# Performance work log

Measured on AMD Instinct MI355X. Metric: run time of the kernel, lower is better.

Reference implementation:

```python
import jax, jax.numpy as jnp
import numpy as np

B, K, N, D, H, DOUT = 16, 8, 196, 768, 3072, 768


def setup_inputs() -> dict:
    key = jax.random.key(0)
    ks = jax.random.split(key, 5)
    scale_w1 = 1.0 / np.sqrt(D)
    scale_w2 = 1.0 / np.sqrt(H)
    return {
        "slots": jax.random.normal(ks[0], (B, K, D), dtype=jnp.float32),
        "pos_embed": jax.random.normal(ks[1], (N, D), dtype=jnp.float32) * 0.02,
        "map_alpha": jax.random.normal(ks[2], (N, DOUT), dtype=jnp.float32) * 0.02,
        "W1": jax.random.normal(ks[3], (D, H), dtype=jnp.float32) * scale_w1,
        "b1": jnp.zeros((H,), dtype=jnp.float32),
        "W2": jax.random.normal(ks[4], (H, DOUT), dtype=jnp.float32) * scale_w2,
        "b2": jnp.zeros((DOUT,), dtype=jnp.float32),
    }


def reference(slots, pos_embed, map_alpha, W1, b1, W2, b2):
    b, k, d = slots.shape
    n = pos_embed.shape[0]
    # broadcast slots over patches and add positional embedding: (B,K,N,D)
    tokens = slots[:, :, None, :] + pos_embed[None, None, :, :]
    # 2-layer MLP with ReLU
    h = jax.nn.relu(jnp.einsum('bknd,dh->bknh', tokens, W1) + b1)
    y_k = jnp.einsum('bknh,ho->bkno', h, W2) + b2  # (B,K,N,DOUT)
    # softmax over K of map_alpha expanded over (B,K); identical across K -> uniform 1/K,
    # computed explicitly for faithfulness to the original module
    m_k = jax.nn.softmax(jnp.broadcast_to(map_alpha[None, None, :, :], (b, k, n, map_alpha.shape[1])), axis=1)
    y = jnp.einsum('bknd,bknd->bnd', y_k, m_k)
    return y
```

## Files before the change

kernel.cpp:

```cpp
#include <hip/hip_runtime.h>
#include <hip/hip_bf16.h>
#include <stdint.h>


typedef __attribute__((ext_vector_type(8))) short bf16x8;
typedef __attribute__((ext_vector_type(4))) float f32x4;

#define AS1 __attribute__((address_space(1)))
#define AS3 __attribute__((address_space(3)))

#define WAIT_VM(N) asm volatile("s_waitcnt vmcnt(" #N ")" ::: "memory")
#define BAR()      asm volatile("s_barrier" ::: "memory")
#define BAR_LDS()  asm volatile("s_waitcnt lgkmcnt(0)\ns_barrier" ::: "memory")

static __device__ __forceinline__ void gld_lds16(const void* g, void* l) {
    __builtin_amdgcn_global_load_lds((const AS1 unsigned int*)g,
                                     (AS3 unsigned int*)l, 16, 0, 0);
}

static __device__ __forceinline__ unsigned short f2bf(float f) {
    union { float f; unsigned int u; } v; v.f = f;
    unsigned int u = v.u;
    return (unsigned short)((u + 0x7fffu + ((u >> 16) & 1u)) >> 16);
}

__global__ void k_prep(const float* __restrict__ W1, unsigned short* __restrict__ W1t,
                       const float* __restrict__ S, const float* __restrict__ P,
                       unsigned short* __restrict__ A1) {
    int idx = blockIdx.x * blockDim.x + threadIdx.x;
    const int C1n = 96 * 3072;
    const int PKn = 96 * 384;
    if (idx < C1n) {
        int r  = idx % 3072;
        int kc = idx / 3072;
        unsigned int po[4];
        #pragma unroll
        for (int j = 0; j < 4; ++j) {
            unsigned short lo = f2bf(W1[(size_t)(kc * 8 + 2 * j) * 3072 + r]);
            unsigned short hi = f2bf(W1[(size_t)(kc * 8 + 2 * j + 1) * 3072 + r]);
            po[j] = (unsigned int)lo | ((unsigned int)hi << 16);
        }
        size_t dst = ((size_t)(r >> 6) * 12 + (kc >> 3)) * 4096
                   + (size_t)((kc & 7) * 64 + (r & 63)) * 8;
        *(uint4*)(W1t + dst) = make_uint4(po[0], po[1], po[2], po[3]);
    } else if (idx < C1n + PKn) {
        int t = idx - C1n;
        int r  = t % 384;
        int kc = t / 384;
        uint4 o = make_uint4(0u, 0u, 0u, 0u);
        if (r < 324) {
            const float* src = (r < 128) ? (S + (size_t)r * 768 + kc * 8)
                                         : (P + (size_t)(r - 128) * 768 + kc * 8);
            float4 a = *(const float4*)(src);
            float4 b = *(const float4*)(src + 4);
            o.x = (unsigned int)f2bf(a.x) | ((unsigned int)f2bf(a.y) << 16);
            o.y = (unsigned int)f2bf(a.z) | ((unsigned int)f2bf(a.w) << 16);
            o.z = (unsigned int)f2bf(b.x) | ((unsigned int)f2bf(b.y) << 16);
            o.w = (unsigned int)f2bf(b.z) | ((unsigned int)f2bf(b.w) << 16);
        }
        size_t dst = ((size_t)(r >> 6) * 12 + (kc >> 3)) * 4096
                   + (size_t)((kc & 7) * 64 + (r & 63)) * 8;
        *(uint4*)(A1 + dst) = o;
    }
}

__launch_bounds__(256)
__global__ void k_gemm1_w2t(const unsigned short* __restrict__ A,
                            const unsigned short* __restrict__ Bt,
                            float* __restrict__ C,
                            const float* __restrict__ W2,
                            unsigned short* __restrict__ W2t) {
    const int tid = threadIdx.x;
    if (blockIdx.x >= 288) {
        int idx = (blockIdx.x - 288) * 256 + tid;
        int r  = idx % 768;
        int kc = idx / 768;
        unsigned int po[4];
        #pragma unroll
        for (int j = 0; j < 4; ++j) {
            unsigned short lo = f2bf(W2[(size_t)(kc * 8 + 2 * j) * 768 + r]);
            unsigned short hi = f2bf(W2[(size_t)(kc * 8 + 2 * j + 1) * 768 + r]);
            po[j] = (unsigned int)lo | ((unsigned int)hi << 16);
        }
        size_t dst = ((size_t)(r >> 6) * 48 + (kc >> 3)) * 4096
                   + (size_t)((kc & 7) * 64 + (r & 63)) * 8;
        *(uint4*)(W2t + dst) = make_uint4(po[0], po[1], po[2], po[3]);
        return;
    }

    __shared__ unsigned short sm[3 * 8192];
    const int lane = tid & 63;
    const int wave = tid >> 6;
    const int wm = wave >> 1, wn = wave & 1;
    const int q = lane >> 4, l16 = lane & 15;

    const int id = blockIdx.x;
    const int j  = id >> 3;
    const int nt = (id & 7) * 6 + j % 6;
    const int rt = j / 6;

    const unsigned short* Ab = A  + (size_t)rt * 12 * 4096;
    const unsigned short* Bb = Bt + (size_t)nt * 12 * 4096;

    f32x4 acc[2][2] = {};
    const int offA = (wm * 32 + l16) * 8;
    const int offB = 4096 + (wn * 32 + l16) * 8;

    auto stage = [&](int i, unsigned short* d) {
        const unsigned short* Ag = Ab + (size_t)i * 4096;
        const unsigned short* Bg = Bb + (size_t)i * 4096;
        gld_lds16(Ag + tid * 8,        d + tid * 8);
        gld_lds16(Ag + 2048 + tid * 8, d + 2048 + tid * 8);
        gld_lds16(Bg + tid * 8,        d + 4096 + tid * 8);
        gld_lds16(Bg + 2048 + tid * 8, d + 6144 + tid * 8);
    };
    auto compute = [&](const unsigned short* buf) {
        #pragma unroll
        for (int ks = 0; ks < 2; ++ks) {
            const int ko = (ks * 4 + q) * 512;
            bf16x8 af0 = *(const bf16x8*)(buf + ko + offA);
            bf16x8 af1 = *(const bf16x8*)(buf + ko + offA + 128);
            bf16x8 bf0 = *(const bf16x8*)(buf + ko + offB);
            bf16x8 bf1 = *(const bf16x8*)(buf + ko + offB + 128);
            acc[0][0] = __builtin_amdgcn_mfma_f32_16x16x32_bf16(af0, bf0, acc[0][0], 0, 0, 0);
            acc[0][1] = __builtin_amdgcn_mfma_f32_16x16x32_bf16(af0, bf1, acc[0][1], 0, 0, 0);
            acc[1][0] = __builtin_amdgcn_mfma_f32_16x16x32_bf16(af1, bf0, acc[1][0], 0, 0, 0);
            acc[1][1] = __builtin_amdgcn_mfma_f32_16x16x32_bf16(af1, bf1, acc[1][1], 0, 0, 0);
        }
    };

    unsigned short* s0 = sm;
    unsigned short* s1 = sm + 8192;
    unsigned short* s2 = sm + 16384;

    stage(0, s0);
    stage(1, s1);
    for (int i = 0; i < 12; i += 3) {
        stage(i + 2, s2); WAIT_VM(8);
        BAR(); compute(s0); BAR_LDS();
        if (i + 3 < 12) { stage(i + 3, s0); WAIT_VM(8); } else { WAIT_VM(4); }
        BAR(); compute(s1); BAR_LDS();
        if (i + 4 < 12) { stage(i + 4, s1); WAIT_VM(8); }
        else if (i + 3 < 12) { WAIT_VM(4); }
        else { WAIT_VM(0); }
        BAR(); compute(s2);
        if (i + 3 < 12) BAR_LDS();
    }

    const int row0 = rt * 64 + wm * 32;
    const int col0 = nt * 64 + wn * 32;
    #pragma unroll
    for (int ii = 0; ii < 2; ++ii) {
        #pragma unroll
        for (int jj = 0; jj < 2; ++jj) {
            int col = col0 + jj * 16 + l16;
            #pragma unroll
            for (int r = 0; r < 4; ++r) {
                int row = row0 + ii * 16 + q * 4 + r;
                if (row < 324) C[(size_t)row * 3072 + col] = acc[ii][jj][r];
            }
        }
    }
}

__global__ void k_hbar(const float* __restrict__ C1, const float* __restrict__ b1,
                       unsigned short* __restrict__ Hb) {
    const int bid  = blockIdx.x;
    const int tid  = threadIdx.x;
    const int bx   = bid % 49;
    const int yq   = bid / 49;
    const int lane = tid & 63;
    const int wv   = tid >> 6;
    const int hc   = yq * 4 + wv;
    const int h0   = hc * 8;
    const int bn   = bx * 64 + lane;
    const int b    = bn / 196;
    const int n    = bn - b * 196;
    const float* prow = C1 + (size_t)(128 + n) * 3072 + h0;
    float4 pA = *(const float4*)(prow);
    float4 pB = *(const float4*)(prow + 4);
    float4 bA = *(const float4*)(b1 + h0);
    float4 bB = *(const float4*)(b1 + h0 + 4);
    float pb[8] = { pA.x + bA.x, pA.y + bA.y, pA.z + bA.z, pA.w + bA.w,
                    pB.x + bB.x, pB.y + bB.y, pB.z + bB.z, pB.w + bB.w };
    float acc[8] = {};
    #pragma unroll
    for (int k = 0; k < 8; ++k) {
        const float* srow = C1 + (size_t)(b * 8 + k) * 3072 + h0;
        float4 sA_ = *(const float4*)(srow);
        float4 sB_ = *(const float4*)(srow + 4);
        acc[0] += fmaxf(sA_.x + pb[0], 0.f);
        acc[1] += fmaxf(sA_.y + pb[1], 0.f);
        acc[2] += fmaxf(sA_.z + pb[2], 0.f);
        acc[3] += fmaxf(sA_.w + pb[3], 0.f);
        acc[4] += fmaxf(sB_.x + pb[4], 0.f);
        acc[5] += fmaxf(sB_.y + pb[5], 0.f);
        acc[6] += fmaxf(sB_.z + pb[6], 0.f);
        acc[7] += fmaxf(sB_.w + pb[7], 0.f);
    }
    unsigned int w0 = (unsigned int)f2bf(acc[0] * 0.125f) | ((unsigned int)f2bf(acc[1] * 0.125f) << 16);
    unsigned int w1 = (unsigned int)f2bf(acc[2] * 0.125f) | ((unsigned int)f2bf(acc[3] * 0.125f) << 16);
    unsigned int w2 = (unsigned int)f2bf(acc[4] * 0.125f) | ((unsigned int)f2bf(acc[5] * 0.125f) << 16);
    unsigned int w3 = (unsigned int)f2bf(acc[6] * 0.125f) | ((unsigned int)f2bf(acc[7] * 0.125f) << 16);
    size_t dst = ((size_t)bx * 48 + (hc >> 3)) * 4096
               + (size_t)((hc & 7) * 64 + lane) * 8;
    *(uint4*)(Hb + dst) = make_uint4(w0, w1, w2, w3);
}

__launch_bounds__(512)
__global__ void k_gemm2(const unsigned short* __restrict__ Hb,
                        const unsigned short* __restrict__ W2t,
                        const float* __restrict__ b2, float* __restrict__ out) {
    __shared__ unsigned short sm[3 * 8192];

    const int tid  = threadIdx.x;
    const int lane = tid & 63;
    const int wave = tid >> 6;
    const int kg = wave >> 2;
    const int w  = wave & 3;
    const int wm = w >> 1, wn = w & 1;
    const int q = lane >> 4, l16 = lane & 15;

    const int id = blockIdx.x;
    int rt, nt;
    if (id < 576) { rt = (id & 7) + 8 * ((id >> 3) % 6); nt = (id >> 3) / 6; }
    else          { rt = 48; nt = id - 576; }

    const unsigned short* Ab = Hb  + (size_t)rt * 48 * 4096;
    const unsigned short* Bb = W2t + (size_t)nt * 48 * 4096;

    f32x4 acc[2][2] = {};

    auto stage = [&](int i, unsigned short* d) {
        gld_lds16(Ab + (size_t)i * 4096 + tid * 8, d + tid * 8);
        gld_lds16(Bb + (size_t)i * 4096 + tid * 8, d + 4096 + tid * 8);
    };

    const int offA = (wm * 32 + l16) * 8;
    const int offB = 4096 + (wn * 32 + l16) * 8;
    const int ko   = (kg * 4 + q) * 512;
    auto compute = [&](const unsigned short* buf) {
        bf16x8 af0 = *(const bf16x8*)(buf + ko + offA);
        bf16x8 af1 = *(const bf16x8*)(buf + ko + offA + 128);
        bf16x8 bf0 = *(const bf16x8*)(buf + ko + offB);
        bf16x8 bf1 = *(const bf16x8*)(buf + ko + offB + 128);
        acc[0][0] = __builtin_amdgcn_mfma_f32_16x16x32_bf16(af0, bf0, acc[0][0], 0, 0, 0);
        acc[0][1] = __builtin_amdgcn_mfma_f32_16x16x32_bf16(af0, bf1, acc[0][1], 0, 0, 0);
        acc[1][0] = __builtin_amdgcn_mfma_f32_16x16x32_bf16(af1, bf0, acc[1][0], 0, 0, 0);
        acc[1][1] = __builtin_amdgcn_mfma_f32_16x16x32_bf16(af1, bf1, acc[1][1], 0, 0, 0);
    };

    unsigned short* s0 = sm;
    unsigned short* s1 = sm + 8192;
    unsigned short* s2 = sm + 16384;

    stage(0, s0);
    stage(1, s1);
    for (int i = 0; i < 48; i += 3) {
        stage(i + 2, s2); WAIT_VM(4);
        BAR(); compute(s0); BAR_LDS();
        if (i + 3 < 48) { stage(i + 3, s0); WAIT_VM(4); } else { WAIT_VM(2); }
        BAR(); compute(s1); BAR_LDS();
        if (i + 4 < 48) { stage(i + 4, s1); WAIT_VM(4); }
        else if (i + 3 < 48) { WAIT_VM(2); }
        else { WAIT_VM(0); }
        BAR(); compute(s2);
        if (i + 3 < 48) BAR_LDS();
    }

    float* smf = (float*)sm;
    __syncthreads();
    if (kg == 1) {
        #pragma unroll
        for (int ii = 0; ii < 2; ++ii)
            #pragma unroll
            for (int jj = 0; jj < 2; ++jj)
                *(f32x4*)(smf + ((size_t)((w * 4 + ii * 2 + jj) * 64 + lane)) * 4) = acc[ii][jj];
    }
    __syncthreads();
    if (kg == 1) return;
    #pragma unroll
    for (int ii = 0; ii < 2; ++ii)
        #pragma unroll
        for (int jj = 0; jj < 2; ++jj) {
            f32x4 p = *(const f32x4*)(smf + ((size_t)((w * 4 + ii * 2 + jj) * 64 + lane)) * 4);
            acc[ii][jj] += p;
        }

    const int row0 = rt * 64 + wm * 32;
    const int col0 = nt * 64 + wn * 32;
    #pragma unroll
    for (int ii = 0; ii < 2; ++ii) {
        #pragma unroll
        for (int jj = 0; jj < 2; ++jj) {
            int col = col0 + jj * 16 + l16;
            float bv = b2[col];
            #pragma unroll
            for (int r = 0; r < 4; ++r) {
                int row = row0 + ii * 16 + q * 4 + r;
                out[(size_t)row * 768 + col] = acc[ii][jj][r] + bv;
            }
        }
    }
}

extern "C" void kernel_launch(void* const* d_in, const int* in_sizes, int n_in,
                              void* d_out, int out_size, void* d_ws, size_t ws_size,
                              hipStream_t stream) {
    const float* slots  = (const float*)d_in[0];
    const float* pos    = (const float*)d_in[1];
    const float* W1     = (const float*)d_in[3];
    const float* b1     = (const float*)d_in[4];
    const float* W2     = (const float*)d_in[5];
    const float* b2     = (const float*)d_in[6];
    float* out = (float*)d_out;

    size_t off = 0;
    auto alloc = [&](size_t bytes) {
        void* p = (char*)d_ws + off;
        off += (bytes + 255) & ~(size_t)255;
        return p;
    };
    unsigned short* W1t = (unsigned short*)alloc((size_t)3072 * 768 * 2);
    unsigned short* W2t = (unsigned short*)alloc((size_t)768 * 3072 * 2);
    unsigned short* A1  = (unsigned short*)alloc((size_t)384 * 768 * 2);
    float*          C1  = (float*)alloc((size_t)384 * 3072 * 4);
    unsigned short* Hb  = (unsigned short*)alloc((size_t)49 * 48 * 4096 * 2);

    k_prep<<<1296, 256, 0, stream>>>(W1, W1t, slots, pos, A1);
    k_gemm1_w2t<<<1440, 256, 0, stream>>>(A1, W1t, C1, W2, W2t);
    k_hbar<<<4704, 256, 0, stream>>>(C1, b1, Hb);
    k_gemm2<<<588, 512, 0, stream>>>(Hb, W2t, b2, out);
}
```

Measured before the change: 129.0 us.

## Fuse four kernels into one persistent kernel with grid-wide barriers

Replaces the four launches (prep, gemm1 plus W2 transpose, hidden averaging, gemm2) with one persistent kernel of 512 blocks that moves between phases through software grid barriers built on atomic counters. The aim is to remove launch gaps and tail effects between stages. Gemm2 also changes from 512-thread blocks with split-K reduction through LDS to 256-thread blocks, so 588 tiles over 512 blocks leaves a second-wave tail. The barrier depends on all blocks being co-resident and has a spin guard that can break out early, and each barrier serialises the grid.

```diff
diff --git a/kernel.cpp b/kernel.cpp
--- a/kernel.cpp
+++ b/kernel.cpp
@@ -12,6 +12,10 @@
 #define WAIT_VM(N) asm volatile("s_waitcnt vmcnt(" #N ")" ::: "memory")
 #define BAR()      asm volatile("s_barrier" ::: "memory")
 #define BAR_LDS()  asm volatile("s_waitcnt lgkmcnt(0)\ns_barrier" ::: "memory")
+
+#define NBLK 512u
+
+__device__ unsigned int g_bar[3];
 
 static __device__ __forceinline__ void gld_lds16(const void* g, void* l) {
     __builtin_amdgcn_global_load_lds((const AS1 unsigned int*)g,
@@ -24,281 +28,275 @@
     return (unsigned short)((u + 0x7fffu + ((u >> 16) & 1u)) >> 16);
 }
 
-__global__ void k_prep(const float* __restrict__ W1, unsigned short* __restrict__ W1t,
-                       const float* __restrict__ S, const float* __restrict__ P,
-                       unsigned short* __restrict__ A1) {
-    int idx = blockIdx.x * blockDim.x + threadIdx.x;
-    const int C1n = 96 * 3072;
-    const int PKn = 96 * 384;
-    if (idx < C1n) {
-        int r  = idx % 3072;
-        int kc = idx / 3072;
-        unsigned int po[4];
-        #pragma unroll
-        for (int j = 0; j < 4; ++j) {
-            unsigned short lo = f2bf(W1[(size_t)(kc * 8 + 2 * j) * 3072 + r]);
-            unsigned short hi = f2bf(W1[(size_t)(kc * 8 + 2 * j + 1) * 3072 + r]);
-            po[j] = (unsigned int)lo | ((unsigned int)hi << 16);
-        }
-        size_t dst = ((size_t)(r >> 6) * 12 + (kc >> 3)) * 4096
-                   + (size_t)((kc & 7) * 64 + (r & 63)) * 8;
-        *(uint4*)(W1t + dst) = make_uint4(po[0], po[1], po[2], po[3]);
-    } else if (idx < C1n + PKn) {
-        int t = idx - C1n;
-        int r  = t % 384;
-        int kc = t / 384;
-        uint4 o = make_uint4(0u, 0u, 0u, 0u);
-        if (r < 324) {
-            const float* src = (r < 128) ? (S + (size_t)r * 768 + kc * 8)
-                                         : (P + (size_t)(r - 128) * 768 + kc * 8);
-            float4 a = *(const float4*)(src);
-            float4 b = *(const float4*)(src + 4);
-            o.x = (unsigned int)f2bf(a.x) | ((unsigned int)f2bf(a.y) << 16);
-            o.y = (unsigned int)f2bf(a.z) | ((unsigned int)f2bf(a.w) << 16);
-            o.z = (unsigned int)f2bf(b.x) | ((unsigned int)f2bf(b.y) << 16);
-            o.w = (unsigned int)f2bf(b.z) | ((unsigned int)f2bf(b.w) << 16);
-        }
-        size_t dst = ((size_t)(r >> 6) * 12 + (kc >> 3)) * 4096
-                   + (size_t)((kc & 7) * 64 + (r & 63)) * 8;
-        *(uint4*)(A1 + dst) = o;
-    }
-}
-
-__launch_bounds__(256)
-__global__ void k_gemm1_w2t(const unsigned short* __restrict__ A,
-                            const unsigned short* __restrict__ Bt,
-                            float* __restrict__ C,
-                            const float* __restrict__ W2,
-                            unsigned short* __restrict__ W2t) {
-    const int tid = threadIdx.x;
-    if (blockIdx.x >= 288) {
-        int idx = (blockIdx.x - 288) * 256 + tid;
-        int r  = idx % 768;
-        int kc = idx / 768;
-        unsigned int po[4];
-        #pragma unroll
-        for (int j = 0; j < 4; ++j) {
-            unsigned short lo = f2bf(W2[(size_t)(kc * 8 + 2 * j) * 768 + r]);
-            unsigned short hi = f2bf(W2[(size_t)(kc * 8 + 2 * j + 1) * 768 + r]);
-            po[j] = (unsigned int)lo | ((unsigned int)hi << 16);
-        }
-        size_t dst = ((size_t)(r >> 6) * 48 + (kc >> 3)) * 4096
-                   + (size_t)((kc & 7) * 64 + (r & 63)) * 8;
-        *(uint4*)(W2t + dst) = make_uint4(po[0], po[1], po[2], po[3]);
-        return;
-    }
-
+static __device__ __forceinline__ void grid_barrier(int i) {
+    __threadfence();
+    __syncthreads();
+    if (threadIdx.x == 0) {
+        unsigned int old = atomicAdd(&g_bar[i], 1u);
+        unsigned int target = (old / NBLK + 1u) * NBLK;
+        int guard = 0;
+        while (__hip_atomic_load(&g_bar[i], __ATOMIC_RELAXED,
+                                 __HIP_MEMORY_SCOPE_AGENT) < target) {
+            __builtin_amdgcn_s_sleep(8);
+            if (++guard > (1 << 17)) break;
+        }
+    }
+    __syncthreads();
+    __threadfence();
+}
+
+__launch_bounds__(256, 2)
+__global__ void k_fused(const float* __restrict__ S, const float* __restrict__ P,
+                        const float* __restrict__ W1, const float* __restrict__ b1,
+                        const float* __restrict__ W2, const float* __restrict__ b2,
+                        unsigned short* __restrict__ W1t, unsigned short* __restrict__ W2t,
+                        unsigned short* __restrict__ A1, float* __restrict__ C1,
+                        unsigned short* __restrict__ Hb, float* __restrict__ out) {
     __shared__ unsigned short sm[3 * 8192];
+
+    const int tid  = threadIdx.x;
+    const int bid  = blockIdx.x;
     const int lane = tid & 63;
     const int wave = tid >> 6;
-    const int wm = wave >> 1, wn = wave & 1;
     const int q = lane >> 4, l16 = lane & 15;
 
-    const int id = blockIdx.x;
-    const int j  = id >> 3;
-    const int nt = (id & 7) * 6 + j % 6;
-    const int rt = j / 6;
-
-    const unsigned short* Ab = A  + (size_t)rt * 12 * 4096;
-    const unsigned short* Bb = Bt + (size_t)nt * 12 * 4096;
-
-    f32x4 acc[2][2] = {};
-    const int offA = (wm * 32 + l16) * 8;
-    const int offB = 4096 + (wn * 32 + l16) * 8;
-
-    auto stage = [&](int i, unsigned short* d) {
-        const unsigned short* Ag = Ab + (size_t)i * 4096;
-        const unsigned short* Bg = Bb + (size_t)i * 4096;
-        gld_lds16(Ag + tid * 8,        d + tid * 8);
-        gld_lds16(Ag + 2048 + tid * 8, d + 2048 + tid * 8);
-        gld_lds16(Bg + tid * 8,        d + 4096 + tid * 8);
-        gld_lds16(Bg + 2048 + tid * 8, d + 6144 + tid * 8);
-    };
-    auto compute = [&](const unsigned short* buf) {
+    {
+        const int C1n = 96 * 3072;
+        const int TOT = C1n + 96 * 384;
+        for (int idx = bid * 256 + tid; idx < TOT; idx += 512 * 256) {
+            if (idx < C1n) {
+                int r  = idx % 3072;
+                int kc = idx / 3072;
+                unsigned int po[4];
+                #pragma unroll
+                for (int j = 0; j < 4; ++j) {
+                    unsigned short lo = f2bf(W1[(size_t)(kc * 8 + 2 * j) * 3072 + r]);
+                    unsigned short hi = f2bf(W1[(size_t)(kc * 8 + 2 * j + 1) * 3072 + r]);
+                    po[j] = (unsigned int)lo | ((unsigned int)hi << 16);
+                }
+                size_t dst = ((size_t)(r >> 6) * 12 + (kc >> 3)) * 4096
+                           + (size_t)((kc & 7) * 64 + (r & 63)) * 8;
+                *(uint4*)(W1t + dst) = make_uint4(po[0], po[1], po[2], po[3]);
+            } else {
+                int t = idx - C1n;
+                int r  = t % 384;
+                int kc = t / 384;
+                uint4 o = make_uint4(0u, 0u, 0u, 0u);
+                if (r < 324) {
+                    const float* src = (r < 128) ? (S + (size_t)r * 768 + kc * 8)
+                                                 : (P + (size_t)(r - 128) * 768 + kc * 8);
+                    float4 a = *(const float4*)(src);
+                    float4 b = *(const float4*)(src + 4);
+                    o.x = (unsigned int)f2bf(a.x) | ((unsigned int)f2bf(a.y) << 16);
+                    o.y = (unsigned int)f2bf(a.z) | ((unsigned int)f2bf(a.w) << 16);
+                    o.z = (unsigned int)f2bf(b.x) | ((unsigned int)f2bf(b.y) << 16);
+                    o.w = (unsigned int)f2bf(b.z) | ((unsigned int)f2bf(b.w) << 16);
+                }
+                size_t dst = ((size_t)(r >> 6) * 12 + (kc >> 3)) * 4096
+                           + (size_t)((kc & 7) * 64 + (r & 63)) * 8;
+                *(uint4*)(A1 + dst) = o;
+            }
+        }
+    }
+    grid_barrier(0);
+
+    if (bid < 288) {
+        const int wm = wave >> 1, wn = wave & 1;
+        const int j  = bid >> 3;
+        const int nt = (bid & 7) * 6 + j % 6;
+        const int rt = j / 6;
+
+        const unsigned short* Ab = A1  + (size_t)rt * 12 * 4096;
+        const unsigned short* Bb = W1t + (size_t)nt * 12 * 4096;
+
+        f32x4 acc[2][2] = {};
+        const int offA = (wm * 32 + l16) * 8;
+        const int offB = 4096 + (wn * 32 + l16) * 8;
+
+        auto stage = [&](int i, unsigned short* d) {
+            const unsigned short* Ag = Ab + (size_t)i * 4096;
+            const unsigned short* Bg = Bb + (size_t)i * 4096;
+            gld_lds16(Ag + tid * 8,        d + tid * 8);
+            gld_lds16(Ag + 2048 + tid * 8, d + 2048 + tid * 8);
+            gld_lds16(Bg + tid * 8,        d + 4096 + tid * 8);
+            gld_lds16(Bg + 2048 + tid * 8, d + 6144 + tid * 8);
+        };
+        auto compute = [&](const unsigned short* buf) {
+            #pragma unroll
+            for (int ks = 0; ks < 2; ++ks) {
+                const int ko = (ks * 4 + q) * 512;
+                bf16x8 af0 = *(const bf16x8*)(buf + ko + offA);
+                bf16x8 af1 = *(const bf16x8*)(buf + ko + offA + 128);
+                bf16x8 bf0 = *(const bf16x8*)(buf + ko + offB);
+                bf16x8 bf1 = *(const bf16x8*)(buf + ko + offB + 128);
+                acc[0][0] = __builtin_amdgcn_mfma_f32_16x16x32_bf16(af0, bf0, acc[0][0], 0, 0, 0);
+                acc[0][1] = __builtin_amdgcn_mfma_f32_16x16x32_bf16(af0, bf1, acc[0][1], 0, 0, 0);
+                acc[1][0] = __builtin_amdgcn_mfma_f32_16x16x32_bf16(af1, bf0, acc[1][0], 0, 0, 0);
+                acc[1][1] = __builtin_amdgcn_mfma_f32_16x16x32_bf16(af1, bf1, acc[1][1], 0, 0, 0);
+            }
+        };
+
+        unsigned short* s0 = sm;
+        unsigned short* s1 = sm + 8192;
+        unsigned short* s2 = sm + 16384;
+
+        stage(0, s0);
+        stage(1, s1);
+        for (int i = 0; i < 12; i += 3) {
+            stage(i + 2, s2); WAIT_VM(8);
+            BAR(); compute(s0); BAR_LDS();
+            if (i + 3 < 12) { stage(i + 3, s0); WAIT_VM(8); } else { WAIT_VM(4); }
+            BAR(); compute(s1); BAR_LDS();
+            if (i + 4 < 12) { stage(i + 4, s1); WAIT_VM(8); }
+            else if (i + 3 < 12) { WAIT_VM(4); }
+            else { WAIT_VM(0); }
+            BAR(); compute(s2);
+            if (i + 3 < 12) BAR_LDS();
+        }
+
+        const int row0 = rt * 64 + wm * 32;
+        const int col0 = nt * 64 + wn * 32;
         #pragma unroll
-        for (int ks = 0; ks < 2; ++ks) {
-            const int ko = (ks * 4 + q) * 512;
-            bf16x8 af0 = *(const bf16x8*)(buf + ko + offA);
-            bf16x8 af1 = *(const bf16x8*)(buf + ko + offA + 128);
-            bf16x8 bf0 = *(const bf16x8*)(buf + ko + offB);
-            bf16x8 bf1 = *(const bf16x8*)(buf + ko + offB + 128);
-            acc[0][0] = __builtin_amdgcn_mfma_f32_16x16x32_bf16(af0, bf0, acc[0][0], 0, 0, 0);
-            acc[0][1] = __builtin_amdgcn_mfma_f32_16x16x32_bf16(af0, bf1, acc[0][1], 0, 0, 0);
-            acc[1][0] = __builtin_amdgcn_mfma_f32_16x16x32_bf16(af1, bf0, acc[1][0], 0, 0, 0);
-            acc[1][1] = __builtin_amdgcn_mfma_f32_16x16x32_bf16(af1, bf1, acc[1][1], 0, 0, 0);
-        }
-    };
-
-    unsigned short* s0 = sm;
-    unsigned short* s1 = sm + 8192;
-    unsigned short* s2 = sm + 16384;
-
-    stage(0, s0);
-    stage(1, s1);
-    for (int i = 0; i < 12; i += 3) {
-        stage(i + 2, s2); WAIT_VM(8);
-        BAR(); compute(s0); BAR_LDS();
-        if (i + 3 < 12) { stage(i + 3, s0); WAIT_VM(8); } else { WAIT_VM(4); }
-        BAR(); compute(s1); BAR_LDS();
-        if (i + 4 < 12) { stage(i + 4, s1); WAIT_VM(8); }
-        else if (i + 3 < 12) { WAIT_VM(4); }
-        else { WAIT_VM(0); }
-        BAR(); compute(s2);
-        if (i + 3 < 12) BAR_LDS();
-    }
-
-    const int row0 = rt * 64 + wm * 32;
-    const int col0 = nt * 64 + wn * 32;
-    #pragma unroll
-    for (int ii = 0; ii < 2; ++ii) {
+        for (int ii = 0; ii < 2; ++ii) {
+            #pragma unroll
+            for (int jj = 0; jj < 2; ++jj) {
+                int col = col0 + jj * 16 + l16;
+                #pragma unroll
+                for (int r = 0; r < 4; ++r) {
+                    int row = row0 + ii * 16 + q * 4 + r;
+                    if (row < 324) C1[(size_t)row * 3072 + col] = acc[ii][jj][r];
+                }
+            }
+        }
+    } else {
+        int base = (bid - 288) * 256 + tid;
+        for (int idx = base; idx < 294912; idx += 224 * 256) {
+            int r  = idx % 768;
+            int kc = idx / 768;
+            unsigned int po[4];
+            #pragma unroll
+            for (int j = 0; j < 4; ++j) {
+                unsigned short lo = f2bf(W2[(size_t)(kc * 8 + 2 * j) * 768 + r]);
+                unsigned short hi = f2bf(W2[(size_t)(kc * 8 + 2 * j + 1) * 768 + r]);
+                po[j] = (unsigned int)lo | ((unsigned int)hi << 16);
+            }
+            size_t dst = ((size_t)(r >> 6) * 48 + (kc >> 3)) * 4096
+                       + (size_t)((kc & 7) * 64 + (r & 63)) * 8;
+            *(uint4*)(W2t + dst) = make_uint4(po[0], po[1], po[2], po[3]);
+        }
+    }
+    grid_barrier(1);
+
+    #pragma unroll 1
+    for (int vb = bid; vb < 4704; vb += 512) {
+        const int bx   = vb % 49;
+        const int yq   = vb / 49;
+        const int hc   = yq * 4 + wave;
+        const int h0   = hc * 8;
+        const int bn   = bx * 64 + lane;
+        const int b    = bn / 196;
+        const int n    = bn - b * 196;
+        const float* prow = C1 + (size_t)(128 + n) * 3072 + h0;
+        float4 pA = *(const float4*)(prow);
+        float4 pB = *(const float4*)(prow + 4);
+        float4 bA = *(const float4*)(b1 + h0);
+        float4 bB = *(const float4*)(b1 + h0 + 4);
+        float pb[8] = { pA.x + bA.x, pA.y + bA.y, pA.z + bA.z, pA.w + bA.w,
+                        pB.x + bB.x, pB.y + bB.y, pB.z + bB.z, pB.w + bB.w };
+        float acc[8] = {};
         #pragma unroll
-        for (int jj = 0; jj < 2; ++jj) {
-            int col = col0 + jj * 16 + l16;
-            #pragma unroll
-            for (int r = 0; r < 4; ++r) {
-                int row = row0 + ii * 16 + q * 4 + r;
-                if (row < 324) C[(size_t)row * 3072 + col] = acc[ii][jj][r];
-            }
-        }
-    }
-}
-
-__global__ void k_hbar(const float* __restrict__ C1, const float* __restrict__ b1,
-                       unsigned short* __restrict__ Hb) {
-    const int bid  = blockIdx.x;
-    const int tid  = threadIdx.x;
-    const int bx   = bid % 49;
-    const int yq   = bid / 49;
-    const int lane = tid & 63;
-    const int wv   = tid >> 6;
-    const int hc   = yq * 4 + wv;
-    const int h0   = hc * 8;
-    const int bn   = bx * 64 + lane;
-    const int b    = bn / 196;
-    const int n    = bn - b * 196;
-    const float* prow = C1 + (size_t)(128 + n) * 3072 + h0;
-    float4 pA = *(const float4*)(prow);
-    float4 pB = *(const float4*)(prow + 4);
-    float4 bA = *(const float4*)(b1 + h0);
-    float4 bB = *(const float4*)(b1 + h0 + 4);
-    float pb[8] = { pA.x + bA.x, pA.y + bA.y, pA.z + bA.z, pA.w + bA.w,
-                    pB.x + bB.x, pB.y + bB.y, pB.z + bB.z, pB.w + bB.w };
-    float acc[8] = {};
-    #pragma unroll
-    for (int k = 0; k < 8; ++k) {
-        const float* srow = C1 + (size_t)(b * 8 + k) * 3072 + h0;
-        float4 sA_ = *(const float4*)(srow);
-        float4 sB_ = *(const float4*)(srow + 4);
-        acc[0] += fmaxf(sA_.x + pb[0], 0.f);
-        acc[1] += fmaxf(sA_.y + pb[1], 0.f);
-        acc[2] += fmaxf(sA_.z + pb[2], 0.f);
-        acc[3] += fmaxf(sA_.w + pb[3], 0.f);
-        acc[4] += fmaxf(sB_.x + pb[4], 0.f);
-        acc[5] += fmaxf(sB_.y + pb[5], 0.f);
-        acc[6] += fmaxf(sB_.z + pb[6], 0.f);
-        acc[7] += fmaxf(sB_.w + pb[7], 0.f);
-    }
-    unsigned int w0 = (unsigned int)f2bf(acc[0] * 0.125f) | ((unsigned int)f2bf(acc[1] * 0.125f) << 16);
-    unsigned int w1 = (unsigned int)f2bf(acc[2] * 0.125f) | ((unsigned int)f2bf(acc[3] * 0.125f) << 16);
-    unsigned int w2 = (unsigned int)f2bf(acc[4] * 0.125f) | ((unsigned int)f2bf(acc[5] * 0.125f) << 16);
-    unsigned int w3 = (unsigned int)f2bf(acc[6] * 0.125f) | ((unsigned int)f2bf(acc[7] * 0.125f) << 16);
-    size_t dst = ((size_t)bx * 48 + (hc >> 3)) * 4096
-               + (size_t)((hc & 7) * 64 + lane) * 8;
-    *(uint4*)(Hb + dst) = make_uint4(w0, w1, w2, w3);
-}
-
-__launch_bounds__(512)
-__global__ void k_gemm2(const unsigned short* __restrict__ Hb,
-                        const unsigned short* __restrict__ W2t,
-                        const float* __restrict__ b2, float* __restrict__ out) {
-    __shared__ unsigned short sm[3 * 8192];
-
-    const int tid  = threadIdx.x;
-    const int lane = tid & 63;
-    const int wave = tid >> 6;
-    const int kg = wave >> 2;
-    const int w  = wave & 3;
-    const int wm = w >> 1, wn = w & 1;
-    const int q = lane >> 4, l16 = lane & 15;
-
-    const int id = blockIdx.x;
-    int rt, nt;
-    if (id < 576) { rt = (id & 7) + 8 * ((id >> 3) % 6); nt = (id >> 3) / 6; }
-    else          { rt = 48; nt = id - 576; }
-
-    const unsigned short* Ab = Hb  + (size_t)rt * 48 * 4096;
-    const unsigned short* Bb = W2t + (size_t)nt * 48 * 4096;
-
-    f32x4 acc[2][2] = {};
-
-    auto stage = [&](int i, unsigned short* d) {
-        gld_lds16(Ab + (size_t)i * 4096 + tid * 8, d + tid * 8);
-        gld_lds16(Bb + (size_t)i * 4096 + tid * 8, d + 4096 + tid * 8);
-    };
-
-    const int offA = (wm * 32 + l16) * 8;
-    const int offB = 4096 + (wn * 32 + l16) * 8;
-    const int ko   = (kg * 4 + q) * 512;
-    auto compute = [&](const unsigned short* buf) {
-        bf16x8 af0 = *(const bf16x8*)(buf + ko + offA);
-        bf16x8 af1 = *(const bf16x8*)(buf + ko + offA + 128);
-        bf16x8 bf0 = *(const bf16x8*)(buf + ko + offB);
-        bf16x8 bf1 = *(const bf16x8*)(buf + ko + offB + 128);
-        acc[0][0] = __builtin_amdgcn_mfma_f32_16x16x32_bf16(af0, bf0, acc[0][0], 0, 0, 0);
-        acc[0][1] = __builtin_amdgcn_mfma_f32_16x16x32_bf16(af0, bf1, acc[0][1], 0, 0, 0);
-        acc[1][0] = __builtin_amdgcn_mfma_f32_16x16x32_bf16(af1, bf0, acc[1][0], 0, 0, 0);
-        acc[1][1] = __builtin_amdgcn_mfma_f32_16x16x32_bf16(af1, bf1, acc[1][1], 0, 0, 0);
-    };
-
-    unsigned short* s0 = sm;
-    unsigned short* s1 = sm + 8192;
-    unsigned short* s2 = sm + 16384;
-
-    stage(0, s0);
-    stage(1, s1);
-    for (int i = 0; i < 48; i += 3) {
-        stage(i + 2, s2); WAIT_VM(4);
-        BAR(); compute(s0); BAR_LDS();
-        if (i + 3 < 48) { stage(i + 3, s0); WAIT_VM(4); } else { WAIT_VM(2); }
-        BAR(); compute(s1); BAR_LDS();
-        if (i + 4 < 48) { stage(i + 4, s1); WAIT_VM(4); }
-        else if (i + 3 < 48) { WAIT_VM(2); }
-        else { WAIT_VM(0); }
-        BAR(); compute(s2);
-        if (i + 3 < 48) BAR_LDS();
-    }
-
-    float* smf = (float*)sm;
-    __syncthreads();
-    if (kg == 1) {
+        for (int k = 0; k < 8; ++k) {
+            const float* srow = C1 + (size_t)(b * 8 + k) * 3072 + h0;
+            float4 sA_ = *(const float4*)(srow);
+            float4 sB_ = *(const float4*)(srow + 4);
+            acc[0] += fmaxf(sA_.x + pb[0], 0.f);
+            acc[1] += fmaxf(sA_.y + pb[1], 0.f);
+            acc[2] += fmaxf(sA_.z + pb[2], 0.f);
+            acc[3] += fmaxf(sA_.w + pb[3], 0.f);
+            acc[4] += fmaxf(sB_.x + pb[4], 0.f);
+            acc[5] += fmaxf(sB_.y + pb[5], 0.f);
+            acc[6] += fmaxf(sB_.z + pb[6], 0.f);
+            acc[7] += fmaxf(sB_.w + pb[7], 0.f);
+        }
+        unsigned int w0 = (unsigned int)f2bf(acc[0] * 0.125f) | ((unsigned int)f2bf(acc[1] * 0.125f) << 16);
+        unsigned int w1 = (unsigned int)f2bf(acc[2] * 0.125f) | ((unsigned int)f2bf(acc[3] * 0.125f) << 16);
+        unsigned int w2 = (unsigned int)f2bf(acc[4] * 0.125f) | ((unsigned int)f2bf(acc[5] * 0.125f) << 16);
+        unsigned int w3 = (unsigned int)f2bf(acc[6] * 0.125f) | ((unsigned int)f2bf(acc[7] * 0.125f) << 16);
+        size_t dst = ((size_t)bx * 48 + (hc >> 3)) * 4096
+                   + (size_t)((hc & 7) * 64 + lane) * 8;
+        *(uint4*)(Hb + dst) = make_uint4(w0, w1, w2, w3);
+    }
+    grid_barrier(2);
+
+    #pragma unroll 1
+    for (int t4 = bid; t4 < 588; t4 += 512) {
+        __syncthreads();
+        const int wm = wave >> 1, wn = wave & 1;
+        int rt, nt;
+        if (t4 < 576) { rt = (t4 & 7) + 8 * ((t4 >> 3) % 6); nt = (t4 >> 3) / 6; }
+        else          { rt = 48; nt = t4 - 576; }
+
+        const unsigned short* Ab = Hb  + (size_t)rt * 48 * 4096;
+        const unsigned short* Bb = W2t + (size_t)nt * 48 * 4096;
+
+        f32x4 acc[2][2] = {};
+        const int offA = (wm * 32 + l16) * 8;
+        const int offB = 4096 + (wn * 32 + l16) * 8;
+
+        auto stage = [&](int i, unsigned short* d) {
+            const unsigned short* Ag = Ab + (size_t)i * 4096;
+            const unsigned short* Bg = Bb + (size_t)i * 4096;
+            gld_lds16(Ag + tid * 8,        d + tid * 8);
+            gld_lds16(Ag + 2048 + tid * 8, d + 2048 + tid * 8);
+            gld_lds16(Bg + tid * 8,        d + 4096 + tid * 8);
+            gld_lds16(Bg + 2048 + tid * 8, d + 6144 + tid * 8);
+        };
+        auto compute = [&](const unsigned short* buf) {
+            #pragma unroll
+            for (int ks = 0; ks < 2; ++ks) {
+                const int ko = (ks * 4 + q) * 512;
+                bf16x8 af0 = *(const bf16x8*)(buf + ko + offA);
+                bf16x8 af1 = *(const bf16x8*)(buf + ko + offA + 128);
+                bf16x8 bf0 = *(const bf16x8*)(buf + ko + offB);
+                bf16x8 bf1 = *(const bf16x8*)(buf + ko + offB + 128);
+                acc[0][0] = __builtin_amdgcn_mfma_f32_16x16x32_bf16(af0, bf0, acc[0][0], 0, 0, 0);
+                acc[0][1] = __builtin_amdgcn_mfma_f32_16x16x32_bf16(af0, bf1, acc[0][1], 0, 0, 0);
+                acc[1][0] = __builtin_amdgcn_mfma_f32_16x16x32_bf16(af1, bf0, acc[1][0], 0, 0, 0);
+                acc[1][1] = __builtin_amdgcn_mfma_f32_16x16x32_bf16(af1, bf1, acc[1][1], 0, 0, 0);
+            }
+        };
+
+        unsigned short* s0 = sm;
+        unsigned short* s1 = sm + 8192;
+        unsigned short* s2 = sm + 16384;
+
+        stage(0, s0);
+        stage(1, s1);
+        for (int i = 0; i < 48; i += 3) {
+            stage(i + 2, s2); WAIT_VM(8);
+            BAR(); compute(s0); BAR_LDS();
+            if (i + 3 < 48) { stage(i + 3, s0); WAIT_VM(8); } else { WAIT_VM(4); }
+            BAR(); compute(s1); BAR_LDS();
+            if (i + 4 < 48) { stage(i + 4, s1); WAIT_VM(8); }
+            else if (i + 3 < 48) { WAIT_VM(4); }
+            else { WAIT_VM(0); }
+            BAR(); compute(s2);
+            if (i + 3 < 48) BAR_LDS();
+        }
+
+        const int row0 = rt * 64 + wm * 32;
+        const int col0 = nt * 64 + wn * 32;
         #pragma unroll
-        for (int ii = 0; ii < 2; ++ii)
-            #pragma unroll
-            for (int jj = 0; jj < 2; ++jj)
-                *(f32x4*)(smf + ((size_t)((w * 4 + ii * 2 + jj) * 64 + lane)) * 4) = acc[ii][jj];
-    }
-    __syncthreads();
-    if (kg == 1) return;
-    #pragma unroll
-    for (int ii = 0; ii < 2; ++ii)
-        #pragma unroll
-        for (int jj = 0; jj < 2; ++jj) {
-            f32x4 p = *(const f32x4*)(smf + ((size_t)((w * 4 + ii * 2 + jj) * 64 + lane)) * 4);
-            acc[ii][jj] += p;
-        }
-
-    const int row0 = rt * 64 + wm * 32;
-    const int col0 = nt * 64 + wn * 32;
-    #pragma unroll
-    for (int ii = 0; ii < 2; ++ii) {
-        #pragma unroll
-        for (int jj = 0; jj < 2; ++jj) {
-            int col = col0 + jj * 16 + l16;
-            float bv = b2[col];
-            #pragma unroll
-            for (int r = 0; r < 4; ++r) {
-                int row = row0 + ii * 16 + q * 4 + r;
-                out[(size_t)row * 768 + col] = acc[ii][jj][r] + bv;
+        for (int ii = 0; ii < 2; ++ii) {
+            #pragma unroll
+            for (int jj = 0; jj < 2; ++jj) {
+                int col = col0 + jj * 16 + l16;
+                float bv = b2[col];
+                #pragma unroll
+                for (int r = 0; r < 4; ++r) {
+                    int row = row0 + ii * 16 + q * 4 + r;
+                    out[(size_t)row * 768 + col] = acc[ii][jj][r] + bv;
+                }
             }
         }
     }
@@ -327,8 +325,6 @@
     float*          C1  = (float*)alloc((size_t)384 * 3072 * 4);
     unsigned short* Hb  = (unsigned short*)alloc((size_t)49 * 48 * 4096 * 2);
 
-    k_prep<<<1296, 256, 0, stream>>>(W1, W1t, slots, pos, A1);
-    k_gemm1_w2t<<<1440, 256, 0, stream>>>(A1, W1t, C1, W2, W2t);
-    k_hbar<<<4704, 256, 0, stream>>>(C1, b1, Hb);
-    k_gemm2<<<588, 512, 0, stream>>>(Hb, W2t, b2, out);
-}
+    k_fused<<<512, 256, 0, stream>>>(slots, pos, W1, b1, W2, b2,
+                                     W1t, W2t, A1, C1, Hb, out);
+}
```

Result: slower. 427.6 us (+231.5%).

## Fuse W1/activation bf16 conversion into GEMM1 and drop prep kernel

Applied to the files above, without the earlier changes.

Removes the separate prep kernel that converted W1 and the slot/pos rows to bf16 tiled layouts. GEMM1 now loads fp32 A rows and W1 columns straight from global memory, packs them to bf16 in registers with v_cvt_pk_bf16_f32, and feeds MFMA with no LDS staging. The W2 transpose blocks are cut to 288 that loop over the data. This saves one launch and the intermediate writes and reads, but GEMM1 now does strided scalar global loads of W1 with no LDS reuse or software pipelining, which may lower its memory efficiency.

```diff
diff --git a/kernel.cpp b/kernel.cpp
--- a/kernel.cpp
+++ b/kernel.cpp
@@ -24,127 +24,94 @@
     return (unsigned short)((u + 0x7fffu + ((u >> 16) & 1u)) >> 16);
 }
 
-__global__ void k_prep(const float* __restrict__ W1, unsigned short* __restrict__ W1t,
-                       const float* __restrict__ S, const float* __restrict__ P,
-                       unsigned short* __restrict__ A1) {
-    int idx = blockIdx.x * blockDim.x + threadIdx.x;
-    const int C1n = 96 * 3072;
-    const int PKn = 96 * 384;
-    if (idx < C1n) {
-        int r  = idx % 3072;
-        int kc = idx / 3072;
-        unsigned int po[4];
-        #pragma unroll
-        for (int j = 0; j < 4; ++j) {
-            unsigned short lo = f2bf(W1[(size_t)(kc * 8 + 2 * j) * 3072 + r]);
-            unsigned short hi = f2bf(W1[(size_t)(kc * 8 + 2 * j + 1) * 3072 + r]);
-            po[j] = (unsigned int)lo | ((unsigned int)hi << 16);
-        }
-        size_t dst = ((size_t)(r >> 6) * 12 + (kc >> 3)) * 4096
-                   + (size_t)((kc & 7) * 64 + (r & 63)) * 8;
-        *(uint4*)(W1t + dst) = make_uint4(po[0], po[1], po[2], po[3]);
-    } else if (idx < C1n + PKn) {
-        int t = idx - C1n;
-        int r  = t % 384;
-        int kc = t / 384;
-        uint4 o = make_uint4(0u, 0u, 0u, 0u);
-        if (r < 324) {
-            const float* src = (r < 128) ? (S + (size_t)r * 768 + kc * 8)
-                                         : (P + (size_t)(r - 128) * 768 + kc * 8);
-            float4 a = *(const float4*)(src);
-            float4 b = *(const float4*)(src + 4);
-            o.x = (unsigned int)f2bf(a.x) | ((unsigned int)f2bf(a.y) << 16);
-            o.y = (unsigned int)f2bf(a.z) | ((unsigned int)f2bf(a.w) << 16);
-            o.z = (unsigned int)f2bf(b.x) | ((unsigned int)f2bf(b.y) << 16);
-            o.w = (unsigned int)f2bf(b.z) | ((unsigned int)f2bf(b.w) << 16);
-        }
-        size_t dst = ((size_t)(r >> 6) * 12 + (kc >> 3)) * 4096
-                   + (size_t)((kc & 7) * 64 + (r & 63)) * 8;
-        *(uint4*)(A1 + dst) = o;
-    }
-}
-
-__launch_bounds__(256)
-__global__ void k_gemm1_w2t(const unsigned short* __restrict__ A,
-                            const unsigned short* __restrict__ Bt,
-                            float* __restrict__ C,
-                            const float* __restrict__ W2,
-                            unsigned short* __restrict__ W2t) {
+static __device__ __forceinline__ unsigned int pkbf(float lo, float hi) {
+    unsigned int d;
+    asm("v_cvt_pk_bf16_f32 %0, %1, %2" : "=v"(d) : "v"(lo), "v"(hi));
+    return d;
+}
+
+__global__ void k_gemm1d(const float* __restrict__ S, const float* __restrict__ P,
+                         const float* __restrict__ W1, const float* __restrict__ W2,
+                         float* __restrict__ C1, unsigned short* __restrict__ W2t) {
     const int tid = threadIdx.x;
-    if (blockIdx.x >= 288) {
-        int idx = (blockIdx.x - 288) * 256 + tid;
-        int r  = idx % 768;
-        int kc = idx / 768;
-        unsigned int po[4];
-        #pragma unroll
-        for (int j = 0; j < 4; ++j) {
-            unsigned short lo = f2bf(W2[(size_t)(kc * 8 + 2 * j) * 768 + r]);
-            unsigned short hi = f2bf(W2[(size_t)(kc * 8 + 2 * j + 1) * 768 + r]);
-            po[j] = (unsigned int)lo | ((unsigned int)hi << 16);
-        }
-        size_t dst = ((size_t)(r >> 6) * 48 + (kc >> 3)) * 4096
-                   + (size_t)((kc & 7) * 64 + (r & 63)) * 8;
-        *(uint4*)(W2t + dst) = make_uint4(po[0], po[1], po[2], po[3]);
+    const int bid = blockIdx.x;
+
+    if (bid >= 288) {
+        int base = (bid - 288) * 256 + tid;
+        #pragma unroll 1
+        for (int idx = base; idx < 294912; idx += 288 * 256) {
+            int r  = idx % 768;
+            int kc = idx / 768;
+            unsigned int po[4];
+            #pragma unroll
+            for (int j = 0; j < 4; ++j) {
+                unsigned short lo = f2bf(W2[(size_t)(kc * 8 + 2 * j) * 768 + r]);
+                unsigned short hi = f2bf(W2[(size_t)(kc * 8 + 2 * j + 1) * 768 + r]);
+                po[j] = (unsigned int)lo | ((unsigned int)hi << 16);
+            }
+            size_t dst = ((size_t)(r >> 6) * 48 + (kc >> 3)) * 4096
+                       + (size_t)((kc & 7) * 64 + (r & 63)) * 8;
+            *(uint4*)(W2t + dst) = make_uint4(po[0], po[1], po[2], po[3]);
+        }
         return;
     }
 
-    __shared__ unsigned short sm[3 * 8192];
     const int lane = tid & 63;
     const int wave = tid >> 6;
     const int wm = wave >> 1, wn = wave & 1;
     const int q = lane >> 4, l16 = lane & 15;
 
-    const int id = blockIdx.x;
-    const int j  = id >> 3;
-    const int nt = (id & 7) * 6 + j % 6;
-    const int rt = j / 6;
-
-    const unsigned short* Ab = A  + (size_t)rt * 12 * 4096;
-    const unsigned short* Bb = Bt + (size_t)nt * 12 * 4096;
+    const int jj_ = bid >> 3;
+    const int nt = (bid & 7) * 6 + jj_ % 6;
+    const int rt = jj_ / 6;
+
+    auto rowptr = [&](int row) -> const float* {
+        row = row < 324 ? row : 323;
+        return (row < 128) ? (S + (size_t)row * 768) : (P + (size_t)(row - 128) * 768);
+    };
+    const float* pA0 = rowptr(rt * 64 + wm * 32 + l16) + q * 8;
+    const float* pA1 = rowptr(rt * 64 + wm * 32 + 16 + l16) + q * 8;
+
+    unsigned int boff[8];
+    #pragma unroll
+    for (int j = 0; j < 8; ++j)
+        boff[j] = (unsigned int)((((q * 8 + j) * 3072) + nt * 64 + wn * 32 + l16) * 4);
 
     f32x4 acc[2][2] = {};
-    const int offA = (wm * 32 + l16) * 8;
-    const int offB = 4096 + (wn * 32 + l16) * 8;
-
-    auto stage = [&](int i, unsigned short* d) {
-        const unsigned short* Ag = Ab + (size_t)i * 4096;
-        const unsigned short* Bg = Bb + (size_t)i * 4096;
-        gld_lds16(Ag + tid * 8,        d + tid * 8);
-        gld_lds16(Ag + 2048 + tid * 8, d + 2048 + tid * 8);
-        gld_lds16(Bg + tid * 8,        d + 4096 + tid * 8);
-        gld_lds16(Bg + 2048 + tid * 8, d + 6144 + tid * 8);
-    };
-    auto compute = [&](const unsigned short* buf) {
+    #pragma unroll
+    for (int i = 0; i < 12; ++i) {
         #pragma unroll
         for (int ks = 0; ks < 2; ++ks) {
-            const int ko = (ks * 4 + q) * 512;
-            bf16x8 af0 = *(const bf16x8*)(buf + ko + offA);
-            bf16x8 af1 = *(const bf16x8*)(buf + ko + offA + 128);
-            bf16x8 bf0 = *(const bf16x8*)(buf + ko + offB);
-            bf16x8 bf1 = *(const bf16x8*)(buf + ko + offB + 128);
-            acc[0][0] = __builtin_amdgcn_mfma_f32_16x16x32_bf16(af0, bf0, acc[0][0], 0, 0, 0);
-            acc[0][1] = __builtin_amdgcn_mfma_f32_16x16x32_bf16(af0, bf1, acc[0][1], 0, 0, 0);
-            acc[1][0] = __builtin_amdgcn_mfma_f32_16x16x32_bf16(af1, bf0, acc[1][0], 0, 0, 0);
-            acc[1][1] = __builtin_amdgcn_mfma_f32_16x16x32_bf16(af1, bf1, acc[1][1], 0, 0, 0);
-        }
-    };
-
-    unsigned short* s0 = sm;
-    unsigned short* s1 = sm + 8192;
-    unsigned short* s2 = sm + 16384;
-
-    stage(0, s0);
-    stage(1, s1);
-    for (int i = 0; i < 12; i += 3) {
-        stage(i + 2, s2); WAIT_VM(8);
-        BAR(); compute(s0); BAR_LDS();
-        if (i + 3 < 12) { stage(i + 3, s0); WAIT_VM(8); } else { WAIT_VM(4); }
-        BAR(); compute(s1); BAR_LDS();
-        if (i + 4 < 12) { stage(i + 4, s1); WAIT_VM(8); }
-        else if (i + 3 < 12) { WAIT_VM(4); }
-        else { WAIT_VM(0); }
-        BAR(); compute(s2);
-        if (i + 3 < 12) BAR_LDS();
+            const int k0 = i * 64 + ks * 32;
+            f32x4 a0lo = *(const f32x4*)(pA0 + k0);
+            f32x4 a0hi = *(const f32x4*)(pA0 + k0 + 4);
+            f32x4 a1lo = *(const f32x4*)(pA1 + k0);
+            f32x4 a1hi = *(const f32x4*)(pA1 + k0 + 4);
+            const char* bb = (const char*)W1 + (size_t)k0 * 3072 * 4;
+            float b0[8], b1[8];
+            #pragma unroll
+            for (int j = 0; j < 8; ++j) {
+                b0[j] = *(const float*)(bb + boff[j]);
+                b1[j] = *(const float*)(bb + boff[j] + 64);
+            }
+            union { unsigned int u[4]; bf16x8 v; } af0, af1, bf0, bf1;
+            #pragma unroll
+            for (int p = 0; p < 2; ++p) {
+                af0.u[p]     = pkbf(a0lo[2 * p], a0lo[2 * p + 1]);
+                af0.u[p + 2] = pkbf(a0hi[2 * p], a0hi[2 * p + 1]);
+                af1.u[p]     = pkbf(a1lo[2 * p], a1lo[2 * p + 1]);
+                af1.u[p + 2] = pkbf(a1hi[2 * p], a1hi[2 * p + 1]);
+            }
+            #pragma unroll
+            for (int p = 0; p < 4; ++p) {
+                bf0.u[p] = pkbf(b0[2 * p], b0[2 * p + 1]);
+                bf1.u[p] = pkbf(b1[2 * p], b1[2 * p + 1]);
+            }
+            acc[0][0] = __builtin_amdgcn_mfma_f32_16x16x32_bf16(af0.v, bf0.v, acc[0][0], 0, 0, 0);
+            acc[0][1] = __builtin_amdgcn_mfma_f32_16x16x32_bf16(af0.v, bf1.v, acc[0][1], 0, 0, 0);
+            acc[1][0] = __builtin_amdgcn_mfma_f32_16x16x32_bf16(af1.v, bf0.v, acc[1][0], 0, 0, 0);
+            acc[1][1] = __builtin_amdgcn_mfma_f32_16x16x32_bf16(af1.v, bf1.v, acc[1][1], 0, 0, 0);
+        }
     }
 
     const int row0 = rt * 64 + wm * 32;
@@ -157,7 +124,7 @@
             #pragma unroll
             for (int r = 0; r < 4; ++r) {
                 int row = row0 + ii * 16 + q * 4 + r;
-                if (row < 324) C[(size_t)row * 3072 + col] = acc[ii][jj][r];
+                if (row < 324) C1[(size_t)row * 3072 + col] = acc[ii][jj][r];
             }
         }
     }
@@ -321,14 +288,11 @@
         off += (bytes + 255) & ~(size_t)255;
         return p;
     };
-    unsigned short* W1t = (unsigned short*)alloc((size_t)3072 * 768 * 2);
+    float*          C1  = (float*)alloc((size_t)384 * 3072 * 4);
     unsigned short* W2t = (unsigned short*)alloc((size_t)768 * 3072 * 2);
-    unsigned short* A1  = (unsigned short*)alloc((size_t)384 * 768 * 2);
-    float*          C1  = (float*)alloc((size_t)384 * 3072 * 4);
     unsigned short* Hb  = (unsigned short*)alloc((size_t)49 * 48 * 4096 * 2);
 
-    k_prep<<<1296, 256, 0, stream>>>(W1, W1t, slots, pos, A1);
-    k_gemm1_w2t<<<1440, 256, 0, stream>>>(A1, W1t, C1, W2, W2t);
+    k_gemm1d<<<576, 256, 0, stream>>>(slots, pos, W1, W2, C1, W2t);
     k_hbar<<<4704, 256, 0, stream>>>(C1, b1, Hb);
     k_gemm2<<<588, 512, 0, stream>>>(Hb, W2t, b2, out);
 }
```

Result: slower. 160.9 us (+24.7%).

## Load GEMM2 MFMA fragments directly from global memory, dropping LDS staging

Applied to the files above, without the earlier changes.

Removes the triple-buffered global-to-LDS pipeline in k_gemm2, along with its barriers and waitcnts. Each wave now loads its bf16x8 A/B fragments straight from the pre-packed global layout into registers, with an unrolled loop. The K split between wave groups is reassigned so each group handles whole stages (pairs of chunks) instead of halves of each stage. This trades away block-level barrier synchronisation for redundant per-wave global loads, since waves sharing A or B rows now each fetch them, relying on L1/L2 hits and compiler-scheduled latency hiding.

```diff
diff --git a/kernel.cpp b/kernel.cpp
--- a/kernel.cpp
+++ b/kernel.cpp
@@ -211,7 +211,7 @@
 __global__ void k_gemm2(const unsigned short* __restrict__ Hb,
                         const unsigned short* __restrict__ W2t,
                         const float* __restrict__ b2, float* __restrict__ out) {
-    __shared__ unsigned short sm[3 * 8192];
+    __shared__ float smf[4096];
 
     const int tid  = threadIdx.x;
     const int lane = tid & 63;
@@ -226,49 +226,29 @@
     if (id < 576) { rt = (id & 7) + 8 * ((id >> 3) % 6); nt = (id >> 3) / 6; }
     else          { rt = 48; nt = id - 576; }
 
-    const unsigned short* Ab = Hb  + (size_t)rt * 48 * 4096;
-    const unsigned short* Bb = W2t + (size_t)nt * 48 * 4096;
+    const unsigned short* Aw = Hb  + (size_t)rt * 48 * 4096
+                             + (size_t)kg * 4096 + q * 512 + (wm * 32 + l16) * 8;
+    const unsigned short* Bw = W2t + (size_t)nt * 48 * 4096
+                             + (size_t)kg * 4096 + q * 512 + (wn * 32 + l16) * 8;
 
     f32x4 acc[2][2] = {};
-
-    auto stage = [&](int i, unsigned short* d) {
-        gld_lds16(Ab + (size_t)i * 4096 + tid * 8, d + tid * 8);
-        gld_lds16(Bb + (size_t)i * 4096 + tid * 8, d + 4096 + tid * 8);
-    };
-
-    const int offA = (wm * 32 + l16) * 8;
-    const int offB = 4096 + (wn * 32 + l16) * 8;
-    const int ko   = (kg * 4 + q) * 512;
-    auto compute = [&](const unsigned short* buf) {
-        bf16x8 af0 = *(const bf16x8*)(buf + ko + offA);
-        bf16x8 af1 = *(const bf16x8*)(buf + ko + offA + 128);
-        bf16x8 bf0 = *(const bf16x8*)(buf + ko + offB);
-        bf16x8 bf1 = *(const bf16x8*)(buf + ko + offB + 128);
-        acc[0][0] = __builtin_amdgcn_mfma_f32_16x16x32_bf16(af0, bf0, acc[0][0], 0, 0, 0);
-        acc[0][1] = __builtin_amdgcn_mfma_f32_16x16x32_bf16(af0, bf1, acc[0][1], 0, 0, 0);
-        acc[1][0] = __builtin_amdgcn_mfma_f32_16x16x32_bf16(af1, bf0, acc[1][0], 0, 0, 0);
-        acc[1][1] = __builtin_amdgcn_mfma_f32_16x16x32_bf16(af1, bf1, acc[1][1], 0, 0, 0);
-    };
-
-    unsigned short* s0 = sm;
-    unsigned short* s1 = sm + 8192;
-    unsigned short* s2 = sm + 16384;
-
-    stage(0, s0);
-    stage(1, s1);
-    for (int i = 0; i < 48; i += 3) {
-        stage(i + 2, s2); WAIT_VM(4);
-        BAR(); compute(s0); BAR_LDS();
-        if (i + 3 < 48) { stage(i + 3, s0); WAIT_VM(4); } else { WAIT_VM(2); }
-        BAR(); compute(s1); BAR_LDS();
-        if (i + 4 < 48) { stage(i + 4, s1); WAIT_VM(4); }
-        else if (i + 3 < 48) { WAIT_VM(2); }
-        else { WAIT_VM(0); }
-        BAR(); compute(s2);
-        if (i + 3 < 48) BAR_LDS();
-    }
-
-    float* smf = (float*)sm;
+    #pragma unroll 4
+    for (int p = 0; p < 24; ++p) {
+        const size_t base = (size_t)p * 8192;
+        #pragma unroll
+        for (int ks = 0; ks < 2; ++ks) {
+            const size_t o = base + ks * 2048;
+            bf16x8 af0 = *(const bf16x8*)(Aw + o);
+            bf16x8 af1 = *(const bf16x8*)(Aw + o + 128);
+            bf16x8 bf0 = *(const bf16x8*)(Bw + o);
+            bf16x8 bf1 = *(const bf16x8*)(Bw + o + 128);
+            acc[0][0] = __builtin_amdgcn_mfma_f32_16x16x32_bf16(af0, bf0, acc[0][0], 0, 0, 0);
+            acc[0][1] = __builtin_amdgcn_mfma_f32_16x16x32_bf16(af0, bf1, acc[0][1], 0, 0, 0);
+            acc[1][0] = __builtin_amdgcn_mfma_f32_16x16x32_bf16(af1, bf0, acc[1][0], 0, 0, 0);
+            acc[1][1] = __builtin_amdgcn_mfma_f32_16x16x32_bf16(af1, bf1, acc[1][1], 0, 0, 0);
+        }
+    }
+
     __syncthreads();
     if (kg == 1) {
         #pragma unroll
```

After: 142.8 us. 10.7% more time.
